# Kernel optimization log

Measured on AMD Instinct MI355X. Metric: run time of the kernel, lower is better.

## Reference

```python
import jax, jax.numpy as jnp
import numpy as np

NUM_HEADS, NUM_KV, HEAD_DIM, WIDTH = 4, 1, 256, 1024
MASK_FILL = -2.3819763e38


def _apply_rope(x, positions, max_wavelength=10000.0):
    # x: [B, T, N, H], positions: [B, T]
    d = x.shape[-1]
    freq_exp = (2.0 / d) * jnp.arange(d // 2, dtype=jnp.float32)
    timescale = max_wavelength ** freq_exp                      # [H/2]
    radians = positions[..., None].astype(jnp.float32) / timescale  # [B, T, H/2]
    radians = radians[..., None, :]                             # [B, T, 1, H/2]
    sin, cos = jnp.sin(radians), jnp.cos(radians)
    x1, x2 = jnp.split(x, 2, axis=-1)
    out = jnp.concatenate([x1 * cos - x2 * sin, x2 * cos + x1 * sin], axis=-1)
    return out.astype(x.dtype)


def _rmsnorm(x, scale):
    var = jnp.mean(jnp.square(x.astype(jnp.float32)), axis=-1, keepdims=True)
    normed = x * jax.lax.rsqrt(var + 1e-6)
    return (normed * (1 + scale)).astype(x.dtype)


def setup_inputs() -> dict:
    key = jax.random.key(0)
    ks = jax.random.split(key, 7)
    B, T, S = 8, 512, 2048
    return {
        "x": jax.random.normal(ks[0], (B, T, WIDTH), jnp.float32),
        "mem_seq": jax.random.normal(ks[1], (B, S, WIDTH), jnp.float32),
        "mem_mask": jax.random.randint(ks[2], (B, S), 0, 2).astype(bool),
        "rms_scale": jax.random.normal(ks[3], (WIDTH,), jnp.float32) * 0.02,
        "q_w": jax.random.normal(ks[4], (NUM_HEADS, WIDTH, HEAD_DIM), jnp.float32) / np.sqrt(WIDTH),
        "kv_w": jax.random.normal(ks[5], (2, NUM_KV, WIDTH, HEAD_DIM), jnp.float32) / np.sqrt(WIDTH),
        "out_w": jax.random.normal(ks[6], (NUM_HEADS, HEAD_DIM, WIDTH), jnp.float32) / np.sqrt(NUM_HEADS * HEAD_DIM),
    }


def reference(x, mem_seq, mem_mask, rms_scale, q_w, kv_w, out_w):
    B, S, _ = mem_seq.shape
    T = x.shape[1]
    G = NUM_HEADS // NUM_KV  # query heads per kv head

    xn = _rmsnorm(x, rms_scale)          # shared RMSNorm params
    mn = _rmsnorm(mem_seq, rms_scale)

    q = jnp.einsum("BTD,NDH->BTNH", xn, q_w)          # [B,T,4,256]
    kv = jnp.einsum("BSD,cKDH->cBSKH", mn, kv_w)      # [2,B,S,1,256]
    k, v = kv[0], kv[1]

    q_pos = jnp.broadcast_to(jnp.arange(S, T + S), (B, T))
    k_pos = jnp.broadcast_to(jnp.arange(S), (B, S))
    q = _apply_rope(q, q_pos) * (HEAD_DIM ** -0.5)
    k = _apply_rope(k, k_pos)

    q = q.reshape(B, T, NUM_KV, G, HEAD_DIM)
    logits = jnp.einsum("BTKGH,BSKH->BKGTS", q, k, preferred_element_type=jnp.float32)
    masked = jnp.where(mem_mask[:, None, None, None, :], logits, MASK_FILL)
    probs = jax.nn.softmax(masked, axis=-1).astype(x.dtype)
    enc = jnp.einsum("BKGTS,BSKH->BTKGH", probs, v).reshape(B, T, NUM_HEADS, HEAD_DIM)
    return jnp.einsum("BTNH,NHD->BTD", enc, out_w)
```

## Files before the change

### kernel.cpp

```cpp
#include <hip/hip_runtime.h>
#include <stdint.h>

typedef __bf16   bf16x8 __attribute__((ext_vector_type(8)));
typedef float    f32x4  __attribute__((ext_vector_type(4)));
typedef float    f32x16 __attribute__((ext_vector_type(16)));
typedef uint16_t u16x8  __attribute__((ext_vector_type(8)));
typedef uint16_t u16x4  __attribute__((ext_vector_type(4)));
typedef uint32_t u32x4  __attribute__((ext_vector_type(4)));

#define DEVFN static __device__ __forceinline__

DEVFN uint16_t f2bf(float f){
  uint32_t u = __builtin_bit_cast(uint32_t, f);
  u += 0x7fffu + ((u >> 16) & 1u);
  return (uint16_t)(u >> 16);
}
DEVFN float bf2f(uint16_t h){
  return __builtin_bit_cast(float, (uint32_t)h << 16);
}
DEVFN bf16x8 ldbf8(const uint16_t* p){
  return __builtin_bit_cast(bf16x8, *(const u16x8*)p);
}
DEVFN void gl16(const void* g, void* l){
  __builtin_amdgcn_global_load_lds((__attribute__((address_space(1))) void*)g,
                                   (__attribute__((address_space(3))) void*)l,
                                   16, 0, 0);
}
DEVFN f32x4 mfma16(bf16x8 a, bf16x8 b, f32x4 c){
  return __builtin_amdgcn_mfma_f32_16x16x32_bf16(a, b, c, 0, 0, 0);
}
DEVFN f32x16 mfma32(bf16x8 a, bf16x8 b, f32x16 c){
  return __builtin_amdgcn_mfma_f32_32x32x16_bf16(a, b, c, 0, 0, 0);
}
DEVFN uint32_t cvtpk(float lo, float hi){
  uint32_t r;
  asm("v_cvt_pk_bf16_f32 %0, %1, %2" : "=v"(r) : "v"(lo), "v"(hi));
  return r;
}
DEVFN void plswap(uint32_t &x, uint32_t &y){
  asm("v_permlane32_swap_b32 %0, %1" : "+v"(x), "+v"(y));
}

__global__ void detect_mask_k(const uint32_t* m, int* flag){
  int i = blockIdx.x * 256 + threadIdx.x;
  uint32_t v = m[i];
  int notint   = (v > 1u) ? 1 : 0;
  int notfloat = (v != 0u && v != 0x3F800000u) ? 2 : 0;
  int bits = notint | notfloat;
  if (__any(bits)){
    int agg = bits;
    agg |= __shfl_xor(agg, 1);  agg |= __shfl_xor(agg, 2);
    agg |= __shfl_xor(agg, 4);  agg |= __shfl_xor(agg, 8);
    agg |= __shfl_xor(agg, 16); agg |= __shfl_xor(agg, 32);
    if ((threadIdx.x & 63) == 0) atomicOr(flag, agg);
  }
}

__global__ void expand_mask_k(const void* m, const int* flag, float* bias){
  int i = blockIdx.x * 256 + threadIdx.x;
  int f = *flag;
  bool on;
  if ((f & 1) == 0)      on = ((const int*)m)[i]   != 0;
  else if ((f & 2) == 0) on = ((const float*)m)[i] != 0.0f;
  else                   on = ((const uint8_t*)m)[i] != 0;
  bias[i] = on ? 0.0f : -1e30f;
}

__global__ __launch_bounds__(256) void rmsnorm_k(const float* __restrict__ x,
                                                 const float* __restrict__ mem,
                                                 uint16_t* __restrict__ xn,
                                                 uint16_t* __restrict__ mn,
                                                 const float* __restrict__ scale){
  int row = blockIdx.x;
  const float* in; uint16_t* out; int r0;
  if (row < 4096){ in = x;  out = xn; r0 = row; }
  else           { in = mem; out = mn; r0 = row - 4096; }
  const float4* ip = (const float4*)(in + (size_t)r0 * 1024);
  float4 v = ip[threadIdx.x];
  float ss = v.x*v.x + v.y*v.y + v.z*v.z + v.w*v.w;
  #pragma unroll
  for (int off = 1; off < 64; off <<= 1) ss += __shfl_xor(ss, off);
  __shared__ float wsum[4];
  if ((threadIdx.x & 63) == 0) wsum[threadIdx.x >> 6] = ss;
  __syncthreads();
  float r = rsqrtf((wsum[0] + wsum[1] + wsum[2] + wsum[3]) * (1.0f/1024.0f) + 1e-6f);
  float4 sc = ((const float4*)scale)[threadIdx.x];
  u16x4 o;
  o[0] = f2bf(v.x * r * (1.0f + sc.x));
  o[1] = f2bf(v.y * r * (1.0f + sc.y));
  o[2] = f2bf(v.z * r * (1.0f + sc.z));
  o[3] = f2bf(v.w * r * (1.0f + sc.w));
  *(u16x4*)(out + (size_t)r0 * 1024 + threadIdx.x * 4) = o;
}

__global__ void transpose_cast_all_k(const float* __restrict__ qw,
                                     const float* __restrict__ kvw,
                                     const float* __restrict__ ow,
                                     uint16_t* __restrict__ wq,
                                     uint16_t* __restrict__ wkv,
                                     uint16_t* __restrict__ wout){
  int z = blockIdx.z;
  const float* in; uint16_t* out; int rs, os, C;
  if (z < 4)      { in = qw  + z*262144;     out = wq  + z*262144;     rs = 256;  os = 1024; C = 256; }
  else if (z < 6) { in = kvw + (z-4)*262144; out = wkv + (z-4)*262144; rs = 256;  os = 1024; C = 256; }
  else            { in = ow;                 out = wout;               rs = 1024; os = 1024; C = 1024; }
  int c0 = blockIdx.x * 32, r0 = blockIdx.y * 32;
  if (c0 >= C) return;
  __shared__ float t[32][33];
  int tx = threadIdx.x, ty = threadIdx.y;
  #pragma unroll
  for (int i = 0; i < 4; ++i)
    t[ty + 8*i][tx] = in[(size_t)(r0 + ty + 8*i) * rs + c0 + tx];
  __syncthreads();
  #pragma unroll
  for (int i = 0; i < 4; ++i)
    out[(size_t)(c0 + ty + 8*i) * os + r0 + tx] = f2bf(t[tx][ty + 8*i]);
}

__global__ __launch_bounds__(256) void rope_all_k(uint16_t* q, uint16_t* kk){
  if (blockIdx.x < 8192){
    int idx = blockIdx.x * 256 + threadIdx.x;
    int j = idx & 127, n = (idx >> 7) & 3, bt = idx >> 9;
    float inv = exp2f((float)j * (-13.287712379549449f / 128.0f));
    float rad = (float)(2048 + (bt & 511)) * inv;
    float s, c; sincosf(rad, &s, &c);
    size_t base = (size_t)bt * 1024 + n * 256 + j;
    float x1 = bf2f(q[base]), x2 = bf2f(q[base + 128]);
    q[base]       = f2bf((x1 * c - x2 * s) * 0.0625f);
    q[base + 128] = f2bf((x2 * c + x1 * s) * 0.0625f);
  } else {
    int idx = (blockIdx.x - 8192) * 256 + threadIdx.x;
    int j = idx & 127, bs = idx >> 7;
    float inv = exp2f((float)j * (-13.287712379549449f / 128.0f));
    float rad = (float)(bs & 2047) * inv;
    float s, c; sincosf(rad, &s, &c);
    size_t base = (size_t)bs * 256 + j;
    float x1 = bf2f(kk[base]), x2 = bf2f(kk[base + 128]);
    kk[base]       = f2bf(x1 * c - x2 * s);
    kk[base + 128] = f2bf(x2 * c + x1 * s);
  }
}

__global__ __launch_bounds__(256) void gemm_qkv_k(const uint16_t* __restrict__ xn,
                                                  const uint16_t* __restrict__ mn,
                                                  const uint16_t* __restrict__ wq,
                                                  const uint16_t* __restrict__ wkv,
                                                  uint16_t* __restrict__ qb,
                                                  uint16_t* __restrict__ kb,
                                                  uint16_t* __restrict__ vt3){
  int bx = blockIdx.x;
  bool isq = bx < 256;
  const uint16_t *A, *Bt;
  int n0, m0, N;
  if (isq){ A = xn; Bt = wq;  n0 = (bx & 7) * 128;  m0 = (bx >> 3) * 128; N = 1024; }
  else    { int b2 = bx - 256; A = mn; Bt = wkv; n0 = (b2 & 3) * 128; m0 = (b2 >> 2) * 128; N = 512; }
  const int K = 1024;
  int tid = threadIdx.x, lane = tid & 63, wid = tid >> 6;
  int wr = wid >> 1, wc = wid & 1;
  int lr = lane & 15, lq = lane >> 4;
  __shared__ __align__(16) uint16_t As[128*32];
  __shared__ __align__(16) uint16_t Bs[128*32];
  f32x4 acc[4][4] = {};
  #pragma unroll 1
  for (int k0 = 0; k0 < K; k0 += 32){
    __syncthreads();
    #pragma unroll
    for (int it = 0; it < 2; ++it){
      int ob = it * 4096 + tid * 16;
      int row = ob >> 6, col = ob & 63;
      gl16((const char*)A  + ((size_t)(m0 + row) * K + k0) * 2 + col,
           (char*)As + it * 4096 + wid * 1024);
      gl16((const char*)Bt + ((size_t)(n0 + row) * K + k0) * 2 + col,
           (char*)Bs + it * 4096 + wid * 1024);
    }
    __syncthreads();
    bf16x8 af[4], bfr[4];
    #pragma unroll
    for (int m = 0; m < 4; ++m)  af[m]  = ldbf8(&As[(wr*64 + m*16 + lr) * 32 + lq * 8]);
    #pragma unroll
    for (int n = 0; n < 4; ++n)  bfr[n] = ldbf8(&Bs[(wc*64 + n*16 + lr) * 32 + lq * 8]);
    #pragma unroll
    for (int m = 0; m < 4; ++m)
      #pragma unroll
      for (int n = 0; n < 4; ++n)
        acc[m][n] = mfma16(af[m], bfr[n], acc[m][n]);
  }
  #pragma unroll
  for (int m = 0; m < 4; ++m)
    #pragma unroll
    for (int n = 0; n < 4; ++n){
      int gr0 = m0 + wr*64 + m*16 + lq*4;
      int gc  = n0 + wc*64 + n*16 + lr;
      if (isq){
        #pragma unroll
        for (int r = 0; r < 4; ++r) qb[(size_t)(gr0 + r) * 1024 + gc] = f2bf(acc[m][n][r]);
      } else if (gc < 256){
        #pragma unroll
        for (int r = 0; r < 4; ++r) kb[(size_t)(gr0 + r) * 256 + gc] = f2bf(acc[m][n][r]);
      } else {
        int h = gc - 256, bb = gr0 >> 11, s0 = gr0 & 2047;
        int st = s0 >> 5, sc = (s0 >> 3) & 3, s8 = s0 & 7;
        u16x4 pk;
        #pragma unroll
        for (int r = 0; r < 4; ++r) pk[r] = f2bf(acc[m][n][r]);
        *(u16x4*)&vt3[((((size_t)bb*64 + st)*4 + sc)*256 + h)*8 + s8] = pk;
      }
    }
}

__global__ __launch_bounds__(256) void gemm_out_k(const uint16_t* __restrict__ A,
                                                  const uint16_t* __restrict__ Bt,
                                                  float* __restrict__ Cf){
  const int N = 1024, K = 1024;
  int n0 = blockIdx.x * 128, m0 = blockIdx.y * 128;
  int tid = threadIdx.x, lane = tid & 63, wid = tid >> 6;
  int wr = wid >> 1, wc = wid & 1;
  int lr = lane & 15, lq = lane >> 4;
  __shared__ __align__(16) uint16_t As[128*32];
  __shared__ __align__(16) uint16_t Bs[128*32];
  f32x4 acc[4][4] = {};
  #pragma unroll 1
  for (int k0 = 0; k0 < K; k0 += 32){
    __syncthreads();
    #pragma unroll
    for (int it = 0; it < 2; ++it){
      int ob = it * 4096 + tid * 16;
      int row = ob >> 6, col = ob & 63;
      gl16((const char*)A  + ((size_t)(m0 + row) * K + k0) * 2 + col,
           (char*)As + it * 4096 + wid * 1024);
      gl16((const char*)Bt + ((size_t)(n0 + row) * K + k0) * 2 + col,
           (char*)Bs + it * 4096 + wid * 1024);
    }
    __syncthreads();
    bf16x8 af[4], bfr[4];
    #pragma unroll
    for (int m = 0; m < 4; ++m)  af[m]  = ldbf8(&As[(wr*64 + m*16 + lr) * 32 + lq * 8]);
    #pragma unroll
    for (int n = 0; n < 4; ++n)  bfr[n] = ldbf8(&Bs[(wc*64 + n*16 + lr) * 32 + lq * 8]);
    #pragma unroll
    for (int m = 0; m < 4; ++m)
      #pragma unroll
      for (int n = 0; n < 4; ++n)
        acc[m][n] = mfma16(af[m], bfr[n], acc[m][n]);
  }
  #pragma unroll
  for (int m = 0; m < 4; ++m)
    #pragma unroll
    for (int n = 0; n < 4; ++n){
      int gr0 = m0 + wr*64 + m*16 + lq*4;
      int gc  = n0 + wc*64 + n*16 + lr;
      #pragma unroll
      for (int r = 0; r < 4; ++r) Cf[(size_t)(gr0 + r) * N + gc] = acc[m][n][r];
    }
}

__global__ __launch_bounds__(512, 2) void attn_k(const uint16_t* __restrict__ Q,
                                                 const uint16_t* __restrict__ Kb,
                                                 const uint16_t* __restrict__ Vt3,
                                                 const float* __restrict__ bias,
                                                 uint16_t* __restrict__ po,
                                                 uint16_t* __restrict__ po3,
                                                 float* __restrict__ pm,
                                                 float* __restrict__ pl){
  int bx = blockIdx.x;
  int b = bx & 7, qt = (bx >> 3) & 7, sh = bx >> 6;
  int tid = threadIdx.x, lane = tid & 63, wid = tid >> 6;
  int n = wid & 3, qs = wid >> 2;
  int lc = lane & 31, hi = lane >> 5;
  __shared__ __align__(16) uint16_t Ks[3*32*256];
  __shared__ __align__(16) uint16_t Vs[3*4*256*8];
  __shared__ uint32_t mask_lds[16];

  int sbeg = sh * 512;
  {
    float bv = bias[b*2048 + sbeg + tid];
    unsigned long long bal = __ballot(bv == 0.0f);
    if (lane == 0){
      mask_lds[wid*2]     = (uint32_t)bal;
      mask_lds[wid*2 + 1] = (uint32_t)(bal >> 32);
    }
  }

  int t0w = qt*64 + qs*32;
  bf16x8 qf[16];
  {
    const uint16_t* qp = Q + (size_t)(b*512 + t0w + lc) * 1024 + n*256 + hi*8;
    #pragma unroll
    for (int kc = 0; kc < 16; ++kc) qf[kc] = ldbf8(qp + kc*16);
  }
  f32x16 o[8] = {};
  float mrow = -1e30f, lrow = 0.0f;

  auto STAGE = [&](int buf, int s0){
    const char* vsrc = (const char*)Vt3 + ((size_t)(b*64 + (s0 >> 5))) * 16384;
    #pragma unroll
    for (int it = 0; it < 2; ++it){
      int ob = it*8192 + tid*16;
      int krow = ob >> 9;
      int kcol = (ob & 511) ^ ((krow & 7) << 4);
      gl16((const char*)Kb + ((size_t)(b*2048 + s0 + krow) * 256) * 2 + kcol,
           (char*)Ks + buf*16384 + it*8192 + wid*1024);
      gl16(vsrc + ob,
           (char*)Vs + buf*16384 + it*8192 + wid*1024);
    }
  };

  STAGE(0, sbeg);
  STAGE(1, sbeg + 32);

  #pragma unroll 1
  for (int t = 0; t < 16; ++t){
    if (t == 0)      asm volatile("s_waitcnt vmcnt(4) lgkmcnt(0)" ::: "memory");
    else if (t < 15) asm volatile("s_waitcnt vmcnt(4)" ::: "memory");
    else             asm volatile("s_waitcnt vmcnt(0)" ::: "memory");
    __builtin_amdgcn_s_barrier();
    asm volatile("" ::: "memory");
    if (t < 14) STAGE((t+2)%3, sbeg + (t+2)*32);

    const uint16_t* ksb = Ks + (t%3)*8192;
    const uint16_t* vsb = Vs + (t%3)*8192;

    f32x16 sacc = {};
    __builtin_amdgcn_s_setprio(1);
    #pragma unroll
    for (int kc = 0; kc < 16; ++kc){
      bf16x8 ak = ldbf8(&ksb[lc*256 + ((kc*16 + hi*8) ^ ((lc & 7) << 3))]);
      sacc = mfma32(ak, qf[kc], sacc);
    }
    __builtin_amdgcn_s_setprio(0);

    uint32_t mw = mask_lds[t];
    int sb4 = hi * 4;
    float p[16];
    float mx = -1e30f;
    #pragma unroll
    for (int r = 0; r < 16; ++r){
      int sr = (r & 3) + 8*(r >> 2) + sb4;
      float v = ((mw >> sr) & 1u) ? sacc[r] : -1e30f;
      p[r] = v;
      mx = fmaxf(mx, v);
    }
    mx = fmaxf(mx, __shfl_xor(mx, 32));
    if (__any(mx > mrow + 8.0f)){
      float mn = fmaxf(mrow, mx);
      float scl = __expf(mrow - mn);
      mrow = mn; lrow *= scl;
      #pragma unroll
      for (int ht = 0; ht < 8; ++ht) o[ht] *= scl;
    }
    float rs = 0.0f;
    #pragma unroll
    for (int r = 0; r < 16; ++r){ p[r] = __expf(p[r] - mrow); rs += p[r]; }
    rs += __shfl_xor(rs, 32);
    lrow += rs;

    uint32_t w0, w1, w2, w3, w4, w5, w6, w7;
    w0 = cvtpk(p[0], p[1]);   w2 = cvtpk(p[4], p[5]);   plswap(w0, w2);
    w1 = cvtpk(p[2], p[3]);   w3 = cvtpk(p[6], p[7]);   plswap(w1, w3);
    w4 = cvtpk(p[8], p[9]);   w6 = cvtpk(p[12], p[13]); plswap(w4, w6);
    w5 = cvtpk(p[10], p[11]); w7 = cvtpk(p[14], p[15]); plswap(w5, w7);
    u32x4 t0v = {w0, w1, w2, w3};
    u32x4 t1v = {w4, w5, w6, w7};
    bf16x8 pa0 = __builtin_bit_cast(bf16x8, t0v);
    bf16x8 pa1 = __builtin_bit_cast(bf16x8, t1v);

    __builtin_amdgcn_s_setprio(1);
    #pragma unroll
    for (int ht = 0; ht < 8; ++ht){
      bf16x8 bv0 = ldbf8(&vsb[(size_t)hi*2048       + (ht*32 + lc)*8]);
      o[ht] = mfma32(pa0, bv0, o[ht]);
      bf16x8 bv1 = ldbf8(&vsb[(size_t)(2 + hi)*2048 + (ht*32 + lc)*8]);
      o[ht] = mfma32(pa1, bv1, o[ht]);
    }
    __builtin_amdgcn_s_setprio(0);
  }

  uint16_t* pop = (sh == 3) ? po3 : po + (size_t)sh * 4194304;
  #pragma unroll
  for (int ht = 0; ht < 8; ++ht)
    #pragma unroll
    for (int r = 0; r < 16; ++r){
      int qr = (r & 3) + 8*(r >> 2) + hi*4;
      pop[(size_t)(b*512 + t0w + qr)*1024 + n*256 + ht*32 + lc] = f2bf(o[ht][r]);
    }
  if (hi == 0){
    int mlidx = sh*16384 + (b*512 + t0w + lc)*4 + n;
    pm[mlidx] = mrow;
    pl[mlidx] = lrow;
  }
}

__global__ __launch_bounds__(64) void merge_k(const uint16_t* __restrict__ po,
                                              const uint16_t* __restrict__ po3,
                                              const float* __restrict__ pm,
                                              const float* __restrict__ pl,
                                              uint16_t* __restrict__ enc){
  int idx = blockIdx.x;
  int row = idx >> 2, n = idx & 3;
  float m = -1e30f;
  #pragma unroll
  for (int h = 0; h < 4; ++h) m = fmaxf(m, pm[h*16384 + idx]);
  float w[4], lsum = 0.0f;
  #pragma unroll
  for (int h = 0; h < 4; ++h){
    w[h] = __expf(pm[h*16384 + idx] - m);
    lsum += pl[h*16384 + idx] * w[h];
  }
  float inv = 1.0f / lsum;
  size_t off = (size_t)row*1024 + n*256 + threadIdx.x*4;
  float acc[4] = {0.f, 0.f, 0.f, 0.f};
  #pragma unroll
  for (int h = 0; h < 4; ++h){
    const uint16_t* src = (h < 3) ? po + (size_t)h*4194304 + off : po3 + off;
    u16x4 a = *(const u16x4*)src;
    #pragma unroll
    for (int r = 0; r < 4; ++r) acc[r] += bf2f(a[r]) * w[h];
  }
  u16x4 ov;
  #pragma unroll
  for (int r = 0; r < 4; ++r) ov[r] = f2bf(acc[r] * inv);
  *(u16x4*)(enc + off) = ov;
}

extern "C" void kernel_launch(void* const* d_in, const int* in_sizes, int n_in,
                              void* d_out, int out_size, void* d_ws, size_t ws_size,
                              hipStream_t stream){
  const float* x    = (const float*)d_in[0];
  const float* mem  = (const float*)d_in[1];
  const void*  mask = d_in[2];
  const float* rms  = (const float*)d_in[3];
  const float* qw   = (const float*)d_in[4];
  const float* kvw  = (const float*)d_in[5];
  const float* ow   = (const float*)d_in[6];
  float* out = (float*)d_out;
  char* ws = (char*)d_ws;

  uint16_t* xn   = (uint16_t*)(ws + 0);
  uint16_t* enc  = (uint16_t*)(ws + 0);
  const size_t MB = 1ull << 20;
  uint16_t* qb   = (uint16_t*)(ws + 8*MB);
  uint16_t* kb   = (uint16_t*)(ws + 16*MB);
  uint16_t* vt3  = (uint16_t*)(ws + 24*MB);
  uint16_t* wq   = (uint16_t*)(ws + 32*MB);
  float*    pm   = (float*)   (ws + 32*MB);
  float*    pl   = (float*)   (ws + 32*MB + 262144);
  uint16_t* wkv  = (uint16_t*)(ws + 34*MB);
  uint16_t* wout = (uint16_t*)(ws + 35*MB);
  float*    bias = (float*)   (ws + 37*MB);
  int*      flag = (int*)     (ws + 37*MB + 65536);
  uint16_t* mn   = (uint16_t*)(ws + 38*MB);
  uint16_t* po   = (uint16_t*)(ws + 38*MB);
  uint16_t* po3  = (uint16_t*)out;

  hipMemsetAsync(flag, 0, 4, stream);
  detect_mask_k<<<16, 256, 0, stream>>>((const uint32_t*)mask, flag);
  expand_mask_k<<<64, 256, 0, stream>>>(mask, flag, bias);

  rmsnorm_k<<<20480, 256, 0, stream>>>(x, mem, xn, mn, rms);

  transpose_cast_all_k<<<dim3(32,32,7), dim3(32,8), 0, stream>>>(qw, kvw, ow, wq, wkv, wout);

  gemm_qkv_k<<<768, 256, 0, stream>>>(xn, mn, wq, wkv, qb, kb, vt3);

  rope_all_k<<<16384, 256, 0, stream>>>(qb, kb);

  attn_k<<<256, 512, 0, stream>>>(qb, kb, vt3, bias, po, po3, pm, pl);
  merge_k<<<16384, 64, 0, stream>>>(po, po3, pm, pl, enc);

  gemm_out_k<<<dim3(8, 32), 256, 0, stream>>>(enc, wout, out);
}
```

Before: 178.4 us.

## Widen GEMM K-tile with swizzled LDS and restructure attention staging to double-buffered 64-key tiles

The GEMM kernels move from a 32-wide K step to a 64-wide K step with XOR-swizzled LDS layout, halving the number of barrier pairs per tile and aiming to reduce bank conflicts. The attention kernel replaces its triple-buffered 32-key pipeline with explicit vmcnt waits by a double-buffered 64-key pipeline using __syncthreads, processing two 32-key subtiles per iteration. This cuts loop iterations and barriers, but the simpler sync may expose more load latency, and the larger LDS footprint can lower occupancy.

```diff
diff --git a/kernel.cpp b/kernel.cpp
--- a/kernel.cpp
+++ b/kernel.cpp
@@ -141,6 +141,48 @@
   }
 }
 
+#define GEMM_BODY(A_, Bt_, K_)                                                  \
+  __shared__ __align__(16) uint16_t As[128*64];                                 \
+  __shared__ __align__(16) uint16_t Bs[128*64];                                 \
+  f32x4 acc[4][4] = {};                                                         \
+  {                                                                             \
+    const int K = (K_);                                                         \
+    _Pragma("unroll 1")                                                         \
+    for (int k0 = 0; k0 < K; k0 += 64){                                         \
+      __syncthreads();                                                          \
+      _Pragma("unroll")                                                         \
+      for (int it = 0; it < 4; ++it){                                           \
+        int ob = it * 4096 + tid * 16;                                          \
+        int row = ob >> 7;                                                      \
+        int col = (ob & 127) ^ ((row & 7) << 4);                                \
+        gl16((const char*)(A_)  + ((size_t)(m0 + row) * K + k0) * 2 + col,      \
+             (char*)As + it * 4096 + wid * 1024);                               \
+        gl16((const char*)(Bt_) + ((size_t)(n0 + row) * K + k0) * 2 + col,      \
+             (char*)Bs + it * 4096 + wid * 1024);                               \
+      }                                                                         \
+      __syncthreads();                                                          \
+      bf16x8 af[2][4], bfr[2][4];                                               \
+      _Pragma("unroll")                                                         \
+      for (int ks = 0; ks < 2; ++ks){                                           \
+        _Pragma("unroll")                                                       \
+        for (int m = 0; m < 4; ++m)                                             \
+          af[ks][m]  = ldbf8(&As[(wr*64 + m*16 + lr) * 64 +                     \
+                                 ((ks*32 + lq*8) ^ ((lr & 7) << 3))]);          \
+        _Pragma("unroll")                                                       \
+        for (int n = 0; n < 4; ++n)                                             \
+          bfr[ks][n] = ldbf8(&Bs[(wc*64 + n*16 + lr) * 64 +                     \
+                                 ((ks*32 + lq*8) ^ ((lr & 7) << 3))]);          \
+      }                                                                         \
+      _Pragma("unroll")                                                         \
+      for (int ks = 0; ks < 2; ++ks)                                            \
+        _Pragma("unroll")                                                       \
+        for (int m = 0; m < 4; ++m)                                             \
+          _Pragma("unroll")                                                     \
+          for (int n = 0; n < 4; ++n)                                           \
+            acc[m][n] = mfma16(af[ks][m], bfr[ks][n], acc[m][n]);               \
+    }                                                                           \
+  }
+
 __global__ __launch_bounds__(256) void gemm_qkv_k(const uint16_t* __restrict__ xn,
                                                   const uint16_t* __restrict__ mn,
                                                   const uint16_t* __restrict__ wq,
@@ -151,40 +193,13 @@
   int bx = blockIdx.x;
   bool isq = bx < 256;
   const uint16_t *A, *Bt;
-  int n0, m0, N;
-  if (isq){ A = xn; Bt = wq;  n0 = (bx & 7) * 128;  m0 = (bx >> 3) * 128; N = 1024; }
-  else    { int b2 = bx - 256; A = mn; Bt = wkv; n0 = (b2 & 3) * 128; m0 = (b2 >> 2) * 128; N = 512; }
-  const int K = 1024;
+  int n0, m0;
+  if (isq){ A = xn; Bt = wq;  n0 = (bx & 7) * 128;  m0 = (bx >> 3) * 128; }
+  else    { int b2 = bx - 256; A = mn; Bt = wkv; n0 = (b2 & 3) * 128; m0 = (b2 >> 2) * 128; }
   int tid = threadIdx.x, lane = tid & 63, wid = tid >> 6;
   int wr = wid >> 1, wc = wid & 1;
   int lr = lane & 15, lq = lane >> 4;
-  __shared__ __align__(16) uint16_t As[128*32];
-  __shared__ __align__(16) uint16_t Bs[128*32];
-  f32x4 acc[4][4] = {};
-  #pragma unroll 1
-  for (int k0 = 0; k0 < K; k0 += 32){
-    __syncthreads();
-    #pragma unroll
-    for (int it = 0; it < 2; ++it){
-      int ob = it * 4096 + tid * 16;
-      int row = ob >> 6, col = ob & 63;
-      gl16((const char*)A  + ((size_t)(m0 + row) * K + k0) * 2 + col,
-           (char*)As + it * 4096 + wid * 1024);
-      gl16((const char*)Bt + ((size_t)(n0 + row) * K + k0) * 2 + col,
-           (char*)Bs + it * 4096 + wid * 1024);
-    }
-    __syncthreads();
-    bf16x8 af[4], bfr[4];
-    #pragma unroll
-    for (int m = 0; m < 4; ++m)  af[m]  = ldbf8(&As[(wr*64 + m*16 + lr) * 32 + lq * 8]);
-    #pragma unroll
-    for (int n = 0; n < 4; ++n)  bfr[n] = ldbf8(&Bs[(wc*64 + n*16 + lr) * 32 + lq * 8]);
-    #pragma unroll
-    for (int m = 0; m < 4; ++m)
-      #pragma unroll
-      for (int n = 0; n < 4; ++n)
-        acc[m][n] = mfma16(af[m], bfr[n], acc[m][n]);
-  }
+  GEMM_BODY(A, Bt, 1024)
   #pragma unroll
   for (int m = 0; m < 4; ++m)
     #pragma unroll
@@ -211,38 +226,11 @@
 __global__ __launch_bounds__(256) void gemm_out_k(const uint16_t* __restrict__ A,
                                                   const uint16_t* __restrict__ Bt,
                                                   float* __restrict__ Cf){
-  const int N = 1024, K = 1024;
   int n0 = blockIdx.x * 128, m0 = blockIdx.y * 128;
   int tid = threadIdx.x, lane = tid & 63, wid = tid >> 6;
   int wr = wid >> 1, wc = wid & 1;
   int lr = lane & 15, lq = lane >> 4;
-  __shared__ __align__(16) uint16_t As[128*32];
-  __shared__ __align__(16) uint16_t Bs[128*32];
-  f32x4 acc[4][4] = {};
-  #pragma unroll 1
-  for (int k0 = 0; k0 < K; k0 += 32){
-    __syncthreads();
-    #pragma unroll
-    for (int it = 0; it < 2; ++it){
-      int ob = it * 4096 + tid * 16;
-      int row = ob >> 6, col = ob & 63;
-      gl16((const char*)A  + ((size_t)(m0 + row) * K + k0) * 2 + col,
-           (char*)As + it * 4096 + wid * 1024);
-      gl16((const char*)Bt + ((size_t)(n0 + row) * K + k0) * 2 + col,
-           (char*)Bs + it * 4096 + wid * 1024);
-    }
-    __syncthreads();
-    bf16x8 af[4], bfr[4];
-    #pragma unroll
-    for (int m = 0; m < 4; ++m)  af[m]  = ldbf8(&As[(wr*64 + m*16 + lr) * 32 + lq * 8]);
-    #pragma unroll
-    for (int n = 0; n < 4; ++n)  bfr[n] = ldbf8(&Bs[(wc*64 + n*16 + lr) * 32 + lq * 8]);
-    #pragma unroll
-    for (int m = 0; m < 4; ++m)
-      #pragma unroll
-      for (int n = 0; n < 4; ++n)
-        acc[m][n] = mfma16(af[m], bfr[n], acc[m][n]);
-  }
+  GEMM_BODY(A, Bt, 1024)
   #pragma unroll
   for (int m = 0; m < 4; ++m)
     #pragma unroll
@@ -250,7 +238,7 @@
       int gr0 = m0 + wr*64 + m*16 + lq*4;
       int gc  = n0 + wc*64 + n*16 + lr;
       #pragma unroll
-      for (int r = 0; r < 4; ++r) Cf[(size_t)(gr0 + r) * N + gc] = acc[m][n][r];
+      for (int r = 0; r < 4; ++r) Cf[(size_t)(gr0 + r) * 1024 + gc] = acc[m][n][r];
     }
 }
 
@@ -267,8 +255,8 @@
   int tid = threadIdx.x, lane = tid & 63, wid = tid >> 6;
   int n = wid & 3, qs = wid >> 2;
   int lc = lane & 31, hi = lane >> 5;
-  __shared__ __align__(16) uint16_t Ks[3*32*256];
-  __shared__ __align__(16) uint16_t Vs[3*4*256*8];
+  __shared__ __align__(16) uint16_t Ks[2*64*256];
+  __shared__ __align__(16) uint16_t Vs[2*2*4*256*8];
   __shared__ uint32_t mask_lds[16];
 
   int sbeg = sh * 512;
@@ -294,85 +282,83 @@
   auto STAGE = [&](int buf, int s0){
     const char* vsrc = (const char*)Vt3 + ((size_t)(b*64 + (s0 >> 5))) * 16384;
     #pragma unroll
-    for (int it = 0; it < 2; ++it){
+    for (int it = 0; it < 4; ++it){
       int ob = it*8192 + tid*16;
       int krow = ob >> 9;
       int kcol = (ob & 511) ^ ((krow & 7) << 4);
       gl16((const char*)Kb + ((size_t)(b*2048 + s0 + krow) * 256) * 2 + kcol,
-           (char*)Ks + buf*16384 + it*8192 + wid*1024);
+           (char*)Ks + buf*32768 + it*8192 + wid*1024);
       gl16(vsrc + ob,
-           (char*)Vs + buf*16384 + it*8192 + wid*1024);
+           (char*)Vs + buf*32768 + it*8192 + wid*1024);
     }
   };
 
   STAGE(0, sbeg);
-  STAGE(1, sbeg + 32);
+  __syncthreads();
 
   #pragma unroll 1
-  for (int t = 0; t < 16; ++t){
-    if (t == 0)      asm volatile("s_waitcnt vmcnt(4) lgkmcnt(0)" ::: "memory");
-    else if (t < 15) asm volatile("s_waitcnt vmcnt(4)" ::: "memory");
-    else             asm volatile("s_waitcnt vmcnt(0)" ::: "memory");
-    __builtin_amdgcn_s_barrier();
-    asm volatile("" ::: "memory");
-    if (t < 14) STAGE((t+2)%3, sbeg + (t+2)*32);
-
-    const uint16_t* ksb = Ks + (t%3)*8192;
-    const uint16_t* vsb = Vs + (t%3)*8192;
-
-    f32x16 sacc = {};
-    __builtin_amdgcn_s_setprio(1);
-    #pragma unroll
-    for (int kc = 0; kc < 16; ++kc){
-      bf16x8 ak = ldbf8(&ksb[lc*256 + ((kc*16 + hi*8) ^ ((lc & 7) << 3))]);
-      sacc = mfma32(ak, qf[kc], sacc);
-    }
-    __builtin_amdgcn_s_setprio(0);
-
-    uint32_t mw = mask_lds[t];
-    int sb4 = hi * 4;
-    float p[16];
-    float mx = -1e30f;
-    #pragma unroll
-    for (int r = 0; r < 16; ++r){
-      int sr = (r & 3) + 8*(r >> 2) + sb4;
-      float v = ((mw >> sr) & 1u) ? sacc[r] : -1e30f;
-      p[r] = v;
-      mx = fmaxf(mx, v);
-    }
-    mx = fmaxf(mx, __shfl_xor(mx, 32));
-    if (__any(mx > mrow + 8.0f)){
-      float mn = fmaxf(mrow, mx);
-      float scl = __expf(mrow - mn);
-      mrow = mn; lrow *= scl;
+  for (int t = 0; t < 8; ++t){
+    if (t < 7) STAGE((t+1) & 1, sbeg + (t+1)*64);
+    #pragma unroll
+    for (int st2 = 0; st2 < 2; ++st2){
+      const uint16_t* ksb = Ks + (t & 1)*16384 + st2*8192;
+      const uint16_t* vsb = Vs + (t & 1)*16384 + st2*8192;
+
+      f32x16 sacc = {};
+      __builtin_amdgcn_s_setprio(1);
       #pragma unroll
-      for (int ht = 0; ht < 8; ++ht) o[ht] *= scl;
-    }
-    float rs = 0.0f;
-    #pragma unroll
-    for (int r = 0; r < 16; ++r){ p[r] = __expf(p[r] - mrow); rs += p[r]; }
-    rs += __shfl_xor(rs, 32);
-    lrow += rs;
-
-    uint32_t w0, w1, w2, w3, w4, w5, w6, w7;
-    w0 = cvtpk(p[0], p[1]);   w2 = cvtpk(p[4], p[5]);   plswap(w0, w2);
-    w1 = cvtpk(p[2], p[3]);   w3 = cvtpk(p[6], p[7]);   plswap(w1, w3);
-    w4 = cvtpk(p[8], p[9]);   w6 = cvtpk(p[12], p[13]); plswap(w4, w6);
-    w5 = cvtpk(p[10], p[11]); w7 = cvtpk(p[14], p[15]); plswap(w5, w7);
-    u32x4 t0v = {w0, w1, w2, w3};
-    u32x4 t1v = {w4, w5, w6, w7};
-    bf16x8 pa0 = __builtin_bit_cast(bf16x8, t0v);
-    bf16x8 pa1 = __builtin_bit_cast(bf16x8, t1v);
-
-    __builtin_amdgcn_s_setprio(1);
-    #pragma unroll
-    for (int ht = 0; ht < 8; ++ht){
-      bf16x8 bv0 = ldbf8(&vsb[(size_t)hi*2048       + (ht*32 + lc)*8]);
-      o[ht] = mfma32(pa0, bv0, o[ht]);
-      bf16x8 bv1 = ldbf8(&vsb[(size_t)(2 + hi)*2048 + (ht*32 + lc)*8]);
-      o[ht] = mfma32(pa1, bv1, o[ht]);
-    }
-    __builtin_amdgcn_s_setprio(0);
+      for (int kc = 0; kc < 16; ++kc){
+        bf16x8 ak = ldbf8(&ksb[lc*256 + ((kc*16 + hi*8) ^ ((lc & 7) << 3))]);
+        sacc = mfma32(ak, qf[kc], sacc);
+      }
+      __builtin_amdgcn_s_setprio(0);
+
+      uint32_t mw = mask_lds[t*2 + st2];
+      int sb4 = hi * 4;
+      float p[16];
+      float mx = -1e30f;
+      #pragma unroll
+      for (int r = 0; r < 16; ++r){
+        int sr = (r & 3) + 8*(r >> 2) + sb4;
+        float v = ((mw >> sr) & 1u) ? sacc[r] : -1e30f;
+        p[r] = v;
+        mx = fmaxf(mx, v);
+      }
+      mx = fmaxf(mx, __shfl_xor(mx, 32));
+      if (__any(mx > mrow + 8.0f)){
+        float mn = fmaxf(mrow, mx);
+        float scl = __expf(mrow - mn);
+        mrow = mn; lrow *= scl;
+        #pragma unroll
+        for (int ht = 0; ht < 8; ++ht) o[ht] *= scl;
+      }
+      float rs = 0.0f;
+      #pragma unroll
+      for (int r = 0; r < 16; ++r){ p[r] = __expf(p[r] - mrow); rs += p[r]; }
+      rs += __shfl_xor(rs, 32);
+      lrow += rs;
+
+      uint32_t w0, w1, w2, w3, w4, w5, w6, w7;
+      w0 = cvtpk(p[0], p[1]);   w2 = cvtpk(p[4], p[5]);   plswap(w0, w2);
+      w1 = cvtpk(p[2], p[3]);   w3 = cvtpk(p[6], p[7]);   plswap(w1, w3);
+      w4 = cvtpk(p[8], p[9]);   w6 = cvtpk(p[12], p[13]); plswap(w4, w6);
+      w5 = cvtpk(p[10], p[11]); w7 = cvtpk(p[14], p[15]); plswap(w5, w7);
+      u32x4 t0v = {w0, w1, w2, w3};
+      u32x4 t1v = {w4, w5, w6, w7};
+      bf16x8 pa0 = __builtin_bit_cast(bf16x8, t0v);
+      bf16x8 pa1 = __builtin_bit_cast(bf16x8, t1v);
+
+      __builtin_amdgcn_s_setprio(1);
+      #pragma unroll
+      for (int ht = 0; ht < 8; ++ht){
+        bf16x8 bv0 = ldbf8(&vsb[(size_t)hi*2048       + (ht*32 + lc)*8]);
+        o[ht] = mfma32(pa0, bv0, o[ht]);
+        bf16x8 bv1 = ldbf8(&vsb[(size_t)(2 + hi)*2048 + (ht*32 + lc)*8]);
+        o[ht] = mfma32(pa1, bv1, o[ht]);
+      }
+      __builtin_amdgcn_s_setprio(0);
+    }
+    __syncthreads();
   }
 
   uint16_t* pop = (sh == 3) ? po3 : po + (size_t)sh * 4194304;
```

After: 181.3 us. No clear change (+1.6%).
